# Performance work log

Measured on AMD Instinct MI355X. Metric: run time of the kernel, lower is better.

Reference implementation:

```python
import jax, jax.numpy as jnp
import numpy as np

DT, TAU_S, TAU_M = 1.0, 4.0, 20.0
ALPHA = float(np.exp(-DT / TAU_S))   # synaptic current decay
BETA = float(np.exp(-DT / TAU_M))    # membrane potential decay
THRESH = 1.0
STEPS, BATCH, D1, D2 = 128, 256, 1024, 1024


def setup_inputs() -> dict:
    key = jax.random.key(0)
    k1, k2 = jax.random.split(key)
    inp = jax.random.uniform(k1, (STEPS, BATCH, D1), dtype=jnp.float32)
    # kaiming_normal_ on (d2, d1): std = sqrt(2 / fan_in), mu = 1.0
    weight = jax.random.normal(k2, (D2, D1), dtype=jnp.float32) * np.sqrt(2.0 / D1)
    return {"input": inp, "weight": weight}


def reference(input, weight):
    steps, batch = input.shape[0], input.shape[1]
    d2 = weight.shape[0]
    # Step i uses input[i-1]; precompute all linear projections at once.
    lin = jnp.einsum('tbi,oi->tbo', input[:-1], weight)  # [steps-1, B, d2]

    def step(carry, cur):
        syn, mem = carry
        # snntorch Synaptic, reset_mechanism='zero': reset from PREVIOUS mem
        reset = (mem > THRESH).astype(mem.dtype)
        syn = ALPHA * syn + cur
        mem = (BETA * mem + syn) * (1.0 - reset)
        spk = (mem > THRESH).astype(mem.dtype)
        return (syn, mem), (spk, mem, syn)

    init = (jnp.zeros((batch, d2), input.dtype), jnp.zeros((batch, d2), input.dtype))
    _, (spk, V, I) = jax.lax.scan(step, init, lin)
    z = jnp.zeros((1, batch, d2), input.dtype)  # step 0 stays zero
    output = jnp.concatenate([z, spk], axis=0)
    V = jnp.concatenate([z, V], axis=0)
    I = jnp.concatenate([z, I], axis=0)
    return output, V, I
```

## Files before the change

### kernel.cpp

```cpp
#include <hip/hip_runtime.h>
#include <hip/hip_fp16.h>


#define STEPS 128
#define BATCH 256
#define DIN   1024
#define DOUT  1024

#define ALPHA 0.7788007830714049f
#define BETA  0.9512294245007140f

constexpr int    GM      = (STEPS - 1) * BATCH;
constexpr size_t PLANE   = (size_t)BATCH * DOUT;
constexpr size_t A_ELEMS = (size_t)GM * DIN;
constexpr size_t W_ELEMS = (size_t)DOUT * DIN;

typedef __attribute__((ext_vector_type(8))) _Float16 half8;
typedef __attribute__((ext_vector_type(4))) float float4v;

__global__ __launch_bounds__(256)
void split_kernel(const float* __restrict__ x,
                  unsigned short* __restrict__ hi,
                  unsigned short* __restrict__ lo)
{
    const size_t i = (size_t)blockIdx.x * 256 + threadIdx.x;
    const float4 v = reinterpret_cast<const float4*>(x)[i];
    float f[4] = {v.x, v.y, v.z, v.w};
    unsigned short hb[4], lb[4];
#pragma unroll
    for (int j = 0; j < 4; ++j) {
        _Float16 h = (_Float16)f[j];
        _Float16 l = (_Float16)(f[j] - (float)h);
        hb[j] = *reinterpret_cast<unsigned short*>(&h);
        lb[j] = *reinterpret_cast<unsigned short*>(&l);
    }
    ushort4 hv = {hb[0], hb[1], hb[2], hb[3]};
    ushort4 lv = {lb[0], lb[1], lb[2], lb[3]};
    reinterpret_cast<ushort4*>(hi)[i] = hv;
    reinterpret_cast<ushort4*>(lo)[i] = lv;
}

__device__ __forceinline__ void load16(const unsigned short* g, unsigned short* l)
{
    __builtin_amdgcn_global_load_lds(
        (const __attribute__((address_space(1))) void*)g,
        (__attribute__((address_space(3))) void*)l, 16, 0, 0);
}

__device__ __forceinline__ half8 ldsr(unsigned addr)
{
    half8 r;
    asm volatile("ds_read_b128 %0, %1" : "=v"(r) : "v"(addr) : "memory");
    return r;
}

#define PHASE_PRE() do {                                        \
    __builtin_amdgcn_s_barrier();                               \
    asm volatile("s_waitcnt lgkmcnt(0)" ::: "memory");          \
    __builtin_amdgcn_sched_barrier(0);                          \
    __builtin_amdgcn_s_setprio(1);                              \
} while (0)

#define PHASE_POST() do {                                       \
    __builtin_amdgcn_s_setprio(0);                              \
    __builtin_amdgcn_sched_barrier(0);                          \
    __builtin_amdgcn_s_barrier();                               \
} while (0)

#define PHASE_POST_VM4() do {                                   \
    __builtin_amdgcn_s_setprio(0);                              \
    __builtin_amdgcn_sched_barrier(0);                          \
    asm volatile("s_waitcnt vmcnt(4)" ::: "memory");            \
    __builtin_amdgcn_s_barrier();                               \
} while (0)

#define MFMA_BLK(MB, BV)                                        \
    _Pragma("unroll")                                           \
    for (int mm = 0; mm < 4; ++mm)                              \
        _Pragma("unroll")                                       \
        for (int nn = 0; nn < 4; ++nn)                          \
            acc[(MB) + mm][nn] = __builtin_amdgcn_mfma_f32_16x16x32_f16( \
                ah[(MB) + mm], BV[nn], acc[(MB) + mm][nn], 0, 0, 0)

__global__ __launch_bounds__(512, 2)
void gemm_kernel(const unsigned short* __restrict__ Ah,
                 const unsigned short* __restrict__ Al,
                 const unsigned short* __restrict__ Wh,
                 const unsigned short* __restrict__ Wl,
                 float* __restrict__ C)
{
    __shared__ __align__(16) unsigned short smem[65536];

    const int lin = blockIdx.x;
    const int xcd = lin & 7, slot = lin >> 3;
    const int mp  = xcd * 16 + (slot >> 2);
    const int nt  = slot & 3;
    if (mp >= GM / 256) return;
    const int m0 = mp * 256;
    const int n0 = nt * 256;

    const int t = threadIdx.x;
    const int w = t >> 6, l = t & 63;
    const int wr = w >> 2, wc = w & 3;
    const int lr = l & 15, q = l >> 4;

    const int swz = q ^ ((l >> 1) & 3);

    const unsigned rdA = (unsigned)((wr * 128 + lr) * 64 + swz * 16);
    const unsigned rdB = (unsigned)(32768 + (wc * 64 + lr) * 64 + swz * 16);

    const int srow = l >> 2;
    const int sg   = ((l & 3) ^ ((l >> 3) & 3)) * 8;

    const size_t sA0 = (size_t)(m0 + w * 32 +      srow) * DIN + sg;
    const size_t sA1 = (size_t)(m0 + w * 32 + 16 + srow) * DIN + sg;
    const size_t sB0 = (size_t)(n0 + w * 32 +      srow) * DIN + sg;
    const size_t sB1 = (size_t)(n0 + w * 32 + 16 + srow) * DIN + sg;

    auto STAGE_H1 = [&](int ks) {
        const int kk = (ks & 31) << 5;
        unsigned short* d = smem + ((ks & 1) << 15) + w * 1024;
        load16(Ah + sA0 + kk, d);
        load16(Ah + sA1 + kk, d + 512);
        load16(Wh + sB0 + kk, d + 16384);
        load16(Wh + sB1 + kk, d + 16896);
    };
    auto STAGE_H2 = [&](int ks) {
        const int kk = (ks & 31) << 5;
        unsigned short* d = smem + ((ks & 1) << 15) + w * 1024;
        load16(Al + sA0 + kk, d + 8192);
        load16(Al + sA1 + kk, d + 8704);
        load16(Wl + sB0 + kk, d + 24576);
        load16(Wl + sB1 + kk, d + 25088);
    };

    float4v acc[8][4];
#pragma unroll
    for (int m = 0; m < 8; ++m)
#pragma unroll
        for (int n = 0; n < 4; ++n)
            acc[m][n] = (float4v){0.f, 0.f, 0.f, 0.f};

    STAGE_H1(0);
    STAGE_H2(0);
    asm volatile("s_waitcnt vmcnt(4)" ::: "memory");
    __builtin_amdgcn_s_barrier();

    for (int kt = 0; kt < 32; ++kt) {
        const unsigned sb = (unsigned)((kt & 1) << 16);
        half8 ah[8], bh[4], bl[4];

#pragma unroll
        for (int m = 0; m < 4; ++m) ah[m] = ldsr(sb + rdA + m * 1024);
#pragma unroll
        for (int n = 0; n < 4; ++n) bh[n] = ldsr(sb + rdB + n * 1024);
        STAGE_H1((kt + 1) & 31);
        PHASE_PRE();  MFMA_BLK(0, bh);  PHASE_POST();

#pragma unroll
        for (int m = 4; m < 8; ++m) ah[m] = ldsr(sb + rdA + m * 1024);
        PHASE_PRE();  MFMA_BLK(4, bh);  PHASE_POST_VM4();

#pragma unroll
        for (int n = 0; n < 4; ++n) bl[n] = ldsr(sb + rdB + 16384 + n * 1024);
        STAGE_H2((kt + 1) & 31);
        PHASE_PRE();  MFMA_BLK(0, bl);  PHASE_POST();

#pragma unroll
        for (int m = 0; m < 4; ++m) ah[m] = ldsr(sb + rdA + 16384 + m * 1024);
        PHASE_PRE();  MFMA_BLK(4, bl);  PHASE_POST();

#pragma unroll
        for (int m = 4; m < 8; ++m) ah[m] = ldsr(sb + rdA + 16384 + m * 1024);
        PHASE_PRE();  MFMA_BLK(0, bh);  PHASE_POST();

        PHASE_PRE();  MFMA_BLK(4, bh);  PHASE_POST_VM4();
    }

    const int mw = m0 + wr * 128 + q * 4;
    const int nw = n0 + wc * 64 + lr;
#pragma unroll
    for (int m = 0; m < 8; ++m)
#pragma unroll
        for (int n = 0; n < 4; ++n)
#pragma unroll
            for (int rg = 0; rg < 4; ++rg)
                C[(size_t)(mw + m * 16 + rg) * DOUT + (nw + n * 16)] = acc[m][n][rg];
}

__global__ __launch_bounds__(256)
void scan_kernel(float* __restrict__ out)
{
    const int idx = blockIdx.x * 256 + threadIdx.x;
    float* o0 = out;
    float* o1 = out + STEPS * PLANE;
    float* o2 = out + 2 * STEPS * PLANE;

    __builtin_nontemporal_store(0.0f, &o0[idx]);
    __builtin_nontemporal_store(0.0f, &o1[idx]);
    __builtin_nontemporal_store(0.0f, &o2[idx]);

    float n1 = o2[idx + PLANE];
    float n2 = o2[idx + 2 * PLANE];
    float n3 = o2[idx + 3 * PLANE];

    float syn = 0.0f, mem = 0.0f;
    size_t off = idx;
    for (int i = 1; i < STEPS; ++i) {
        off += PLANE;
        const float cur = n1; n1 = n2; n2 = n3;
        if (i + 3 < STEPS) n3 = o2[off + 3 * PLANE];
        const float reset = (mem > 1.0f) ? 1.0f : 0.0f;
        syn = ALPHA * syn + cur;
        mem = (BETA * mem + syn) * (1.0f - reset);
        const float spk = (mem > 1.0f) ? 1.0f : 0.0f;
        __builtin_nontemporal_store(spk, &o0[off]);
        __builtin_nontemporal_store(mem, &o1[off]);
        __builtin_nontemporal_store(syn, &o2[off]);
    }
}

extern "C" void kernel_launch(void* const* d_in, const int* in_sizes, int n_in,
                              void* d_out, int out_size, void* d_ws, size_t ws_size,
                              hipStream_t stream)
{
    const float* input  = (const float*)d_in[0];
    const float* weight = (const float*)d_in[1];
    float* out = (float*)d_out;

    unsigned short* Ah = (unsigned short*)out;
    unsigned short* Al = Ah + A_ELEMS;
    unsigned short* Wh = (unsigned short*)(out + STEPS * PLANE);
    unsigned short* Wl = Wh + W_ELEMS;
    float* lin = out + 2 * STEPS * PLANE + PLANE;

    split_kernel<<<(int)(A_ELEMS / 1024), 256, 0, stream>>>(input, Ah, Al);
    split_kernel<<<(int)(W_ELEMS / 1024), 256, 0, stream>>>(weight, Wh, Wl);

    gemm_kernel<<<512, 512, 0, stream>>>(Ah, Al, Wh, Wl, lin);

    scan_kernel<<<(int)(PLANE / 256), 256, 0, stream>>>(out);
}
```

Before: 682.9 us.

## Fuse fp16 hi/lo split of input into GEMM A-tile staging

Removes the separate split pass over the large input activation. The GEMM now loads fp32 A rows straight into registers, splits each value into fp16 hi and lo parts, and writes both into LDS. The weight split pass and its async LDS loads stay as before. This drops a full write and re-read of the split A copy through global memory. In exchange the GEMM reads twice as many A bytes, spends VALU work on conversion, and waits on vmcnt(0) at every k-step, which may weaken load/compute overlap.

```diff
diff --git a/kernel.cpp b/kernel.cpp
--- a/kernel.cpp
+++ b/kernel.cpp
@@ -12,7 +12,6 @@
 
 constexpr int    GM      = (STEPS - 1) * BATCH;
 constexpr size_t PLANE   = (size_t)BATCH * DOUT;
-constexpr size_t A_ELEMS = (size_t)GM * DIN;
 constexpr size_t W_ELEMS = (size_t)DOUT * DIN;
 
 typedef __attribute__((ext_vector_type(8))) _Float16 half8;
@@ -64,13 +63,6 @@
 #define PHASE_POST() do {                                       \
     __builtin_amdgcn_s_setprio(0);                              \
     __builtin_amdgcn_sched_barrier(0);                          \
-    __builtin_amdgcn_s_barrier();                               \
-} while (0)
-
-#define PHASE_POST_VM4() do {                                   \
-    __builtin_amdgcn_s_setprio(0);                              \
-    __builtin_amdgcn_sched_barrier(0);                          \
-    asm volatile("s_waitcnt vmcnt(4)" ::: "memory");            \
     __builtin_amdgcn_s_barrier();                               \
 } while (0)
 
@@ -83,8 +75,7 @@
                 ah[(MB) + mm], BV[nn], acc[(MB) + mm][nn], 0, 0, 0)
 
 __global__ __launch_bounds__(512, 2)
-void gemm_kernel(const unsigned short* __restrict__ Ah,
-                 const unsigned short* __restrict__ Al,
+void gemm_kernel(const float* __restrict__ Af,
                  const unsigned short* __restrict__ Wh,
                  const unsigned short* __restrict__ Wl,
                  float* __restrict__ C)
@@ -110,30 +101,37 @@
     const unsigned rdB = (unsigned)(32768 + (wc * 64 + lr) * 64 + swz * 16);
 
     const int srow = l >> 2;
-    const int sg   = ((l & 3) ^ ((l >> 3) & 3)) * 8;
-
-    const size_t sA0 = (size_t)(m0 + w * 32 +      srow) * DIN + sg;
-    const size_t sA1 = (size_t)(m0 + w * 32 + 16 + srow) * DIN + sg;
-    const size_t sB0 = (size_t)(n0 + w * 32 +      srow) * DIN + sg;
-    const size_t sB1 = (size_t)(n0 + w * 32 + 16 + srow) * DIN + sg;
-
-    auto STAGE_H1 = [&](int ks) {
+    const int sgE  = ((l & 3) ^ ((l >> 3) & 3)) * 8;
+
+    const size_t fA0 = (size_t)(m0 + w * 32 +      srow) * DIN + sgE;
+    const size_t fA1 = (size_t)(m0 + w * 32 + 16 + srow) * DIN + sgE;
+    const size_t sB0 = (size_t)(n0 + w * 32 +      srow) * DIN + sgE;
+    const size_t sB1 = (size_t)(n0 + w * 32 + 16 + srow) * DIN + sgE;
+
+    const unsigned dstA = (unsigned)(w * 1024 + l * 8);
+
+    auto STAGE_W = [&](int ks) {
         const int kk = (ks & 31) << 5;
         unsigned short* d = smem + ((ks & 1) << 15) + w * 1024;
-        load16(Ah + sA0 + kk, d);
-        load16(Ah + sA1 + kk, d + 512);
         load16(Wh + sB0 + kk, d + 16384);
         load16(Wh + sB1 + kk, d + 16896);
-    };
-    auto STAGE_H2 = [&](int ks) {
-        const int kk = (ks & 31) << 5;
-        unsigned short* d = smem + ((ks & 1) << 15) + w * 1024;
-        load16(Al + sA0 + kk, d + 8192);
-        load16(Al + sA1 + kk, d + 8704);
         load16(Wl + sB0 + kk, d + 24576);
         load16(Wl + sB1 + kk, d + 25088);
     };
 
+    auto WRITE_A = [&](float4 x, float4 y, unsigned short* ds, unsigned off) {
+        float f[8] = {x.x, x.y, x.z, x.w, y.x, y.y, y.z, y.w};
+        half8 h, lo8;
+#pragma unroll
+        for (int j = 0; j < 8; ++j) {
+            _Float16 hh = (_Float16)f[j];
+            h[j]   = hh;
+            lo8[j] = (_Float16)(f[j] - (float)hh);
+        }
+        *reinterpret_cast<half8*>(ds + dstA + off)        = h;
+        *reinterpret_cast<half8*>(ds + dstA + off + 8192) = lo8;
+    };
+
     float4v acc[8][4];
 #pragma unroll
     for (int m = 0; m < 8; ++m)
@@ -141,29 +139,41 @@
         for (int n = 0; n < 4; ++n)
             acc[m][n] = (float4v){0.f, 0.f, 0.f, 0.f};
 
-    STAGE_H1(0);
-    STAGE_H2(0);
-    asm volatile("s_waitcnt vmcnt(4)" ::: "memory");
-    __builtin_amdgcn_s_barrier();
+    {
+        float4 a0 = *reinterpret_cast<const float4*>(Af + fA0);
+        float4 a1 = *reinterpret_cast<const float4*>(Af + fA0 + 4);
+        float4 a2 = *reinterpret_cast<const float4*>(Af + fA1);
+        float4 a3 = *reinterpret_cast<const float4*>(Af + fA1 + 4);
+        STAGE_W(0);
+        unsigned short* ds = smem;
+        WRITE_A(a0, a1, ds, 0);
+        WRITE_A(a2, a3, ds, 512);
+        asm volatile("s_waitcnt vmcnt(0) lgkmcnt(0)" ::: "memory");
+        __builtin_amdgcn_s_barrier();
+    }
 
     for (int kt = 0; kt < 32; ++kt) {
         const unsigned sb = (unsigned)((kt & 1) << 16);
+        const int kn = ((kt + 1) & 31) << 5;
         half8 ah[8], bh[4], bl[4];
 
+        float4 a0 = *reinterpret_cast<const float4*>(Af + fA0 + kn);
+        float4 a1 = *reinterpret_cast<const float4*>(Af + fA0 + kn + 4);
+        float4 a2 = *reinterpret_cast<const float4*>(Af + fA1 + kn);
+        float4 a3 = *reinterpret_cast<const float4*>(Af + fA1 + kn + 4);
 #pragma unroll
         for (int m = 0; m < 4; ++m) ah[m] = ldsr(sb + rdA + m * 1024);
 #pragma unroll
         for (int n = 0; n < 4; ++n) bh[n] = ldsr(sb + rdB + n * 1024);
-        STAGE_H1((kt + 1) & 31);
         PHASE_PRE();  MFMA_BLK(0, bh);  PHASE_POST();
 
 #pragma unroll
         for (int m = 4; m < 8; ++m) ah[m] = ldsr(sb + rdA + m * 1024);
-        PHASE_PRE();  MFMA_BLK(4, bh);  PHASE_POST_VM4();
+        PHASE_PRE();  MFMA_BLK(4, bh);  PHASE_POST();
 
 #pragma unroll
         for (int n = 0; n < 4; ++n) bl[n] = ldsr(sb + rdB + 16384 + n * 1024);
-        STAGE_H2((kt + 1) & 31);
+        STAGE_W((kt + 1) & 31);
         PHASE_PRE();  MFMA_BLK(0, bl);  PHASE_POST();
 
 #pragma unroll
@@ -174,7 +184,16 @@
         for (int m = 4; m < 8; ++m) ah[m] = ldsr(sb + rdA + 16384 + m * 1024);
         PHASE_PRE();  MFMA_BLK(0, bh);  PHASE_POST();
 
-        PHASE_PRE();  MFMA_BLK(4, bh);  PHASE_POST_VM4();
+        PHASE_PRE();  MFMA_BLK(4, bh);
+        __builtin_amdgcn_s_setprio(0);
+        __builtin_amdgcn_sched_barrier(0);
+        {
+            unsigned short* ds = smem + (((kt + 1) & 1) << 15);
+            WRITE_A(a0, a1, ds, 0);
+            WRITE_A(a2, a3, ds, 512);
+        }
+        asm volatile("s_waitcnt vmcnt(0) lgkmcnt(0)" ::: "memory");
+        __builtin_amdgcn_s_barrier();
     }
 
     const int mw = m0 + wr * 128 + q * 4;
@@ -228,16 +247,13 @@
     const float* weight = (const float*)d_in[1];
     float* out = (float*)d_out;
 
-    unsigned short* Ah = (unsigned short*)out;
-    unsigned short* Al = Ah + A_ELEMS;
     unsigned short* Wh = (unsigned short*)(out + STEPS * PLANE);
     unsigned short* Wl = Wh + W_ELEMS;
     float* lin = out + 2 * STEPS * PLANE + PLANE;
 
-    split_kernel<<<(int)(A_ELEMS / 1024), 256, 0, stream>>>(input, Ah, Al);
     split_kernel<<<(int)(W_ELEMS / 1024), 256, 0, stream>>>(weight, Wh, Wl);
 
-    gemm_kernel<<<512, 512, 0, stream>>>(Ah, Al, Wh, Wl, lin);
+    gemm_kernel<<<512, 512, 0, stream>>>(input, Wh, Wl, lin);
 
     scan_kernel<<<(int)(PLANE / 256), 256, 0, stream>>>(out);
 }
```

Measured after the change: 629.7 us. 1.08x faster.
